# Optimization experiments

Hardware: AMD Instinct MI355X
Metric: run time of the kernel (lower is better)

## Reference

```python
import jax, jax.numpy as jnp
import numpy as np

D_MODEL = 1024
D_FF = 4096
N_EXPERTS = 8
TEMPERATURE = 1.0


def setup_inputs() -> dict:
    key = jax.random.key(0)
    ks = jax.random.split(key, 12)
    s_in = 1.0 / np.sqrt(D_MODEL)
    s_ff = 1.0 / np.sqrt(D_FF)
    return {
        "h": jax.random.normal(ks[0], (2, 2048, D_MODEL), dtype=jnp.float32),
        "Wr": jax.random.normal(ks[1], (D_MODEL, N_EXPERTS), dtype=jnp.float32) * s_in,
        "br": jnp.zeros((N_EXPERTS,), dtype=jnp.float32),
        "We1": jax.random.normal(ks[2], (N_EXPERTS, D_MODEL, D_FF), dtype=jnp.float32) * s_in,
        "be1": jnp.zeros((N_EXPERTS, D_FF), dtype=jnp.float32),
        "We2": jax.random.normal(ks[3], (N_EXPERTS, D_FF, D_MODEL), dtype=jnp.float32) * s_ff,
        "be2": jnp.zeros((N_EXPERTS, D_MODEL), dtype=jnp.float32),
        "Ws1": jax.random.normal(ks[4], (D_MODEL, D_FF), dtype=jnp.float32) * s_in,
        "bs1": jnp.zeros((D_FF,), dtype=jnp.float32),
        "Ws2": jax.random.normal(ks[5], (D_FF, D_MODEL), dtype=jnp.float32) * s_ff,
        "bs2": jnp.zeros((D_MODEL,), dtype=jnp.float32),
        "top_k": 2,
    }


def reference(h, Wr, br, We1, be1, We2, be2, Ws1, bs1, Ws2, bs2, top_k):
    # router: Linear -> temperature-scaled softmax over experts
    gate = jax.nn.softmax((h @ Wr + br) / max(1e-06, TEMPERATURE), axis=-1)  # [b,s,E]
    k = min(int(top_k), gate.shape[-1])
    vals, idx = jax.lax.top_k(gate, k)  # [b,s,k]

    # dense all-expert FFN (matches the original mask-multiply semantics)
    hid = jax.nn.gelu(jnp.einsum('bsd,edf->ebsf', h, We1) + be1[:, None, None, :])
    eout = jnp.einsum('ebsf,efd->ebsd', hid, We2) + be2[:, None, None, :]  # [E,b,s,d]

    # per-expert combine weight: sum over top-k slots of val * onehot(idx)
    onehot = jax.nn.one_hot(idx, gate.shape[-1], dtype=h.dtype)  # [b,s,k,E]
    w_e = jnp.einsum('bsk,bske->bse', vals, onehot)  # [b,s,E]
    out = jnp.einsum('bse,ebsd->bsd', w_e, eout)

    # shared FFN residual branch
    out = out + (jax.nn.gelu(h @ Ws1 + bs1) @ Ws2 + bs2)
    gate_mean = jnp.mean(gate)
    return (out, gate_mean)
```

## Files before the change

### kernel.cpp

```cpp
#include <hip/hip_runtime.h>
#include <hip/hip_bf16.h>
#include <cstdint>
#include <cstddef>

#define NTOK   4096
#define DMODEL 1024
#define DFF    4096
#define NEXP   8
#define ROWCAP 13312
#define MTILES 104

typedef __attribute__((ext_vector_type(8))) short short8;
typedef __attribute__((ext_vector_type(4))) float float4v;

__device__ __forceinline__ unsigned short f2bf(float f) {
    unsigned u = __builtin_bit_cast(unsigned, f);
    u = (u + 0x7fffu + ((u >> 16) & 1u)) >> 16;
    return (unsigned short)u;
}

__device__ __forceinline__ float gelu_f(float x) {
    float u = 0.7978845608028654f * x * (1.f + 0.044715f * x * x);
    float e = __expf(2.f * u);
    return x * (1.f - 1.f / (e + 1.f));
}

__device__ __forceinline__ void gl_lds16(const unsigned short* g, unsigned short* l) {
    __builtin_amdgcn_global_load_lds((const __attribute__((address_space(1))) void*)g,
                                     (__attribute__((address_space(3))) void*)l, 16, 0, 0);
}

__global__ __launch_bounds__(256) void router_k(const float* __restrict__ h,
                                                const float* __restrict__ Wr,
                                                const float* __restrict__ br,
                                                int* __restrict__ meta,
                                                int* __restrict__ slot_e,
                                                int* __restrict__ slot_pos,
                                                float* __restrict__ slot_v,
                                                unsigned short* __restrict__ Xbf,
                                                float* __restrict__ out) {
    __shared__ float wr_s[16 * 516];
    const int tid = threadIdx.x;
    for (int i = tid; i < 8192; i += 256) {
        int j = i >> 3, e = i & 7;
        wr_s[(j >> 6) * 516 + (j & 63) * 8 + e] = Wr[i];
    }
    __syncthreads();
    const int tok = blockIdx.x * 16 + (tid >> 4);
    const int part = tid & 15;
    const float* hp = h + (size_t)tok * DMODEL + part * 64;
    unsigned short* xp = Xbf + (size_t)tok * DMODEL + part * 64;
    const float* wbase = &wr_s[part * 516];
    float acc8[8] = {0.f, 0.f, 0.f, 0.f, 0.f, 0.f, 0.f, 0.f};
    #pragma unroll
    for (int j4 = 0; j4 < 16; j4++) {
        float4v hv = *(const float4v*)(hp + j4 * 4);
        ushort4 o;
        o.x = f2bf(hv[0]); o.y = f2bf(hv[1]); o.z = f2bf(hv[2]); o.w = f2bf(hv[3]);
        *(ushort4*)(xp + j4 * 4) = o;
        #pragma unroll
        for (int jj = 0; jj < 4; jj++) {
            const float* wr = wbase + (j4 * 4 + jj) * 8;
            float4v w0 = *(const float4v*)wr;
            float4v w1 = *(const float4v*)(wr + 4);
            #pragma unroll
            for (int e = 0; e < 4; e++) {
                acc8[e]     = fmaf(hv[jj], w0[e], acc8[e]);
                acc8[e + 4] = fmaf(hv[jj], w1[e], acc8[e + 4]);
            }
        }
    }
    #pragma unroll
    for (int e = 0; e < 8; e++) {
        acc8[e] += __shfl_xor(acc8[e], 1);
        acc8[e] += __shfl_xor(acc8[e], 2);
        acc8[e] += __shfl_xor(acc8[e], 4);
        acc8[e] += __shfl_xor(acc8[e], 8);
    }
    if (part == 0) {
        float p[8];
        float mx = -1e30f;
        #pragma unroll
        for (int e = 0; e < 8; e++) { p[e] = acc8[e] + br[e]; mx = fmaxf(mx, p[e]); }
        float s = 0.f;
        #pragma unroll
        for (int e = 0; e < 8; e++) { p[e] = __expf(p[e] - mx); s += p[e]; }
        float inv = 1.f / s;
        #pragma unroll
        for (int e = 0; e < 8; e++) p[e] *= inv;
        int i1 = 0;
        #pragma unroll
        for (int q = 1; q < 8; q++) if (p[q] > p[i1]) i1 = q;
        int i2 = (i1 == 0) ? 1 : 0;
        #pragma unroll
        for (int q = 0; q < 8; q++) if (q != i1 && p[q] > p[i2]) i2 = q;
        int pos1 = atomicAdd(&meta[i1], 1);
        int pos2 = atomicAdd(&meta[i2], 1);
        slot_e[tok * 2] = i1;     slot_e[tok * 2 + 1] = i2;
        slot_pos[tok * 2] = pos1; slot_pos[tok * 2 + 1] = pos2;
        slot_v[tok * 2] = p[i1];  slot_v[tok * 2 + 1] = p[i2];
    }
    if (blockIdx.x == 0 && tid == 0) out[(size_t)NTOK * DMODEL] = 0.125f;
}

__global__ __launch_bounds__(256) void meta_init(int* __restrict__ meta,
                                                 int* __restrict__ row_token,
                                                 float* __restrict__ row_weight) {
    int i = blockIdx.x * 256 + threadIdx.x;
    if (i < ROWCAP) { row_token[i] = 0; row_weight[i] = 0.f; }
    if (blockIdx.x == 0 && threadIdx.x == 0) {
        int rb = 0;
        meta[8] = 0;
        for (int g = 0; g < 8; g++) {
            rb += ((meta[g] + 127) >> 7) << 7;
            meta[9 + g] = rb;
        }
        meta[17] = rb + NTOK;
    }
}

__global__ __launch_bounds__(256) void scatter_k(const int* __restrict__ meta,
                                                 const int* __restrict__ slot_e,
                                                 const int* __restrict__ slot_pos,
                                                 const float* __restrict__ slot_v,
                                                 int* __restrict__ row_token,
                                                 float* __restrict__ row_weight) {
    int idx = blockIdx.x * 256 + threadIdx.x;
    if (idx < NTOK * 2) {
        int e = slot_e[idx];
        int row = meta[8 + e] + slot_pos[idx];
        row_token[row] = idx >> 1;
        row_weight[row] = slot_v[idx];
    } else if (idx < NTOK * 3) {
        int t = idx - NTOK * 2;
        row_token[meta[16] + t] = t;
        row_weight[meta[16] + t] = 1.0f;
    }
}

__global__ __launch_bounds__(256) void wtrans(const float* __restrict__ Wexp,
                                              const float* __restrict__ Wsh,
                                              unsigned short* __restrict__ dst,
                                              int K, int N) {
    const int g = blockIdx.z;
    const float* src = (g < 8) ? (Wexp + (size_t)g * K * N) : Wsh;
    unsigned short* d = dst + (size_t)g * K * N;
    const int n0 = blockIdx.x * 64, k0 = blockIdx.y * 64;
    __shared__ float t[64 * 65];
    const int r = threadIdx.x >> 4, c4 = (threadIdx.x & 15) * 4;
    #pragma unroll
    for (int i = 0; i < 4; i++) {
        float4v v = *(const float4v*)(src + (size_t)(k0 + r + i * 16) * N + n0 + c4);
        float* tp = &t[(r + i * 16) * 65 + c4];
        tp[0] = v[0]; tp[1] = v[1]; tp[2] = v[2]; tp[3] = v[3];
    }
    __syncthreads();
    const int nn = threadIdx.x >> 3, kc = (threadIdx.x & 7) * 8;
    #pragma unroll
    for (int p = 0; p < 2; p++) {
        int n = p * 32 + nn;
        unsigned short o[8];
        #pragma unroll
        for (int j = 0; j < 8; j++) o[j] = f2bf(t[(kc + j) * 65 + n]);
        *(uint4*)(d + (size_t)(n0 + n) * K + k0 + kc) = *(const uint4*)o;
    }
}

template <int MODE>
__global__ __launch_bounds__(256) void gemm_moe(
    const unsigned short* __restrict__ A,
    const unsigned short* __restrict__ WT,
    const float* __restrict__ bexp,
    const float* __restrict__ bsh,
    unsigned short* __restrict__ HidOut,
    float* __restrict__ Out,
    const int* __restrict__ meta,
    const int* __restrict__ row_token,
    const float* __restrict__ row_weight) {
    constexpr int K = (MODE == 1) ? DMODEL : DFF;
    constexpr int N = (MODE == 1) ? DFF : DMODEL;
    const int n0 = blockIdx.x * 128;
    const int row0 = blockIdx.y * 128;

    __shared__ int rb[10];
    __shared__ unsigned short sm[17408];

    if (threadIdx.x < 10) rb[threadIdx.x] = meta[8 + threadIdx.x];
    __syncthreads();
    if (row0 >= rb[9]) return;
    int g = 0;
    #pragma unroll
    for (int q = 0; q < 8; q++) if (row0 >= rb[q + 1]) g = q + 1;
    const unsigned short* __restrict__ BT = WT + (size_t)g * K * N;
    const float* __restrict__ bias = (g < 8) ? (bexp + (size_t)g * N) : bsh;

    const int tid = threadIdx.x;
    const int wave = tid >> 6, lane = tid & 63;
    const int lrow8 = lane >> 3, kst = lane & 7;
    const int swz = kst ^ lrow8;
    const int wm = wave & 1, wn = wave >> 1;
    const int lr = lane & 15, quad = lane >> 4, l7 = lr & 7;

    const unsigned short* ag[4];
    const unsigned short* bg[4];
    unsigned short* al[4];
    unsigned short* bl[4];
    #pragma unroll
    for (int s = 0; s < 4; s++) {
        int seg = wave * 4 + s;
        int row = seg * 8 + lrow8;
        size_t arow = (MODE == 1) ? (size_t)row_token[row0 + row] : (size_t)(row0 + row);
        ag[s] = A + arow * K + swz * 8;
        bg[s] = BT + (size_t)(n0 + row) * K + swz * 8;
        al[s] = &sm[seg * 512];
        bl[s] = &sm[8192 + seg * 512];
    }

    float4v acc[4][4];
    #pragma unroll
    for (int i = 0; i < 4; i++)
        #pragma unroll
        for (int j = 0; j < 4; j++) acc[i][j] = (float4v){0.f, 0.f, 0.f, 0.f};

    for (int kb = 0; kb < K; kb += 64) {
        #pragma unroll
        for (int s = 0; s < 4; s++) gl_lds16(ag[s] + kb, al[s]);
        #pragma unroll
        for (int s = 0; s < 4; s++) gl_lds16(bg[s] + kb, bl[s]);
        __syncthreads();
        #pragma unroll
        for (int ks = 0; ks < 2; ks++) {
            const int koff = ((ks * 4 + quad) ^ l7) * 8;
            short8 af[4], bf[4];
            #pragma unroll
            for (int mi = 0; mi < 4; mi++)
                af[mi] = *(const short8*)&sm[(wm * 64 + mi * 16 + lr) * 64 + koff];
            #pragma unroll
            for (int ni = 0; ni < 4; ni++)
                bf[ni] = *(const short8*)&sm[8192 + (wn * 64 + ni * 16 + lr) * 64 + koff];
            #pragma unroll
            for (int mi = 0; mi < 4; mi++)
                #pragma unroll
                for (int ni = 0; ni < 4; ni++)
                    acc[mi][ni] = __builtin_amdgcn_mfma_f32_16x16x32_bf16(
                        af[mi], bf[ni], acc[mi][ni], 0, 0, 0);
        }
        __syncthreads();
    }

    if (MODE == 1) {
        #pragma unroll
        for (int ni = 0; ni < 4; ni++) {
            int col = wn * 64 + ni * 16 + lr;
            float b = bias[n0 + col];
            #pragma unroll
            for (int mi = 0; mi < 4; mi++) {
                int rowb = wm * 64 + mi * 16 + quad * 4;
                #pragma unroll
                for (int r2 = 0; r2 < 4; r2++)
                    sm[(rowb + r2) * 136 + col] = f2bf(gelu_f(acc[mi][ni][r2] + b));
            }
        }
        __syncthreads();
        const int row = tid >> 1, half = tid & 1;
        const unsigned short* srcp = &sm[row * 136 + half * 64];
        unsigned short* dstp = &HidOut[(size_t)(row0 + row) * DFF + n0 + half * 64];
        #pragma unroll
        for (int j = 0; j < 8; j++)
            *(uint4*)(dstp + j * 8) = *(const uint4*)(srcp + j * 8);
    } else {
        #pragma unroll
        for (int mi = 0; mi < 4; mi++) {
            int rbase = row0 + wm * 64 + mi * 16 + quad * 4;
            int tok[4]; float w[4];
            #pragma unroll
            for (int r2 = 0; r2 < 4; r2++) {
                tok[r2] = row_token[rbase + r2];
                w[r2] = row_weight[rbase + r2];
            }
            #pragma unroll
            for (int ni = 0; ni < 4; ni++) {
                int col = n0 + wn * 64 + ni * 16 + lr;
                float b = bias[col];
                #pragma unroll
                for (int r2 = 0; r2 < 4; r2++) {
                    if (w[r2] != 0.f)
                        atomicAdd(&Out[(size_t)tok[r2] * DMODEL + col],
                                  w[r2] * (acc[mi][ni][r2] + b));
                }
            }
        }
    }
}

extern "C" void kernel_launch(void* const* d_in, const int* in_sizes, int n_in,
                              void* d_out, int out_size, void* d_ws, size_t ws_size,
                              hipStream_t stream) {
    const float* h   = (const float*)d_in[0];
    const float* Wr  = (const float*)d_in[1];
    const float* br  = (const float*)d_in[2];
    const float* We1 = (const float*)d_in[3];
    const float* be1 = (const float*)d_in[4];
    const float* We2 = (const float*)d_in[5];
    const float* be2 = (const float*)d_in[6];
    const float* Ws1 = (const float*)d_in[7];
    const float* bs1 = (const float*)d_in[8];
    const float* Ws2 = (const float*)d_in[9];
    const float* bs2 = (const float*)d_in[10];
    float* out = (float*)d_out;

    char* ws = (char*)d_ws;
    int* meta         = (int*)ws;
    int* slot_e       = (int*)(ws + 4096);
    int* slot_pos     = (int*)(ws + 36864);
    float* slot_v     = (float*)(ws + 69632);
    int* row_token    = (int*)(ws + 102400);
    float* row_weight = (float*)(ws + 155648);
    unsigned short* Xbf = (unsigned short*)(ws + (1ull << 20));
    unsigned short* WT  = (unsigned short*)(ws + (16ull << 20));
    unsigned short* Hid = (unsigned short*)(ws + (96ull << 20));

    hipMemsetAsync(meta, 0, 256, stream);
    hipMemsetAsync(d_out, 0, sizeof(float) * (size_t)out_size, stream);
    router_k<<<NTOK / 16, 256, 0, stream>>>(h, Wr, br, meta, slot_e, slot_pos, slot_v, Xbf, out);
    meta_init<<<ROWCAP / 256, 256, 0, stream>>>(meta, row_token, row_weight);
    scatter_k<<<(NTOK * 3) / 256, 256, 0, stream>>>(meta, slot_e, slot_pos, slot_v,
                                                    row_token, row_weight);
    wtrans<<<dim3(DFF / 64, DMODEL / 64, 9), 256, 0, stream>>>(We1, Ws1, WT, DMODEL, DFF);
    gemm_moe<1><<<dim3(DFF / 128, MTILES), 256, 0, stream>>>(
        Xbf, WT, be1, bs1, Hid, nullptr, meta, row_token, row_weight);
    wtrans<<<dim3(DMODEL / 64, DFF / 64, 9), 256, 0, stream>>>(We2, Ws2, WT, DFF, DMODEL);
    gemm_moe<2><<<dim3(DMODEL / 128, MTILES), 256, 0, stream>>>(
        Hid, WT, be2, bs2, nullptr, out, meta, row_token, row_weight);
}
```

Baseline: 779.2 us.

## Load GEMM fragments directly from global with panel-packed weights and split-K

Result: slower. 1.310 ms (+68.1%).

```diff
diff --git a/kernel.cpp b/kernel.cpp
--- a/kernel.cpp
+++ b/kernel.cpp
@@ -23,11 +23,6 @@
     float u = 0.7978845608028654f * x * (1.f + 0.044715f * x * x);
     float e = __expf(2.f * u);
     return x * (1.f - 1.f / (e + 1.f));
-}
-
-__device__ __forceinline__ void gl_lds16(const unsigned short* g, unsigned short* l) {
-    __builtin_amdgcn_global_load_lds((const __attribute__((address_space(1))) void*)g,
-                                     (__attribute__((address_space(3))) void*)l, 16, 0, 0);
 }
 
 __global__ __launch_bounds__(256) void router_k(const float* __restrict__ h,
@@ -156,18 +151,19 @@
     }
     __syncthreads();
     const int nn = threadIdx.x >> 3, kc = (threadIdx.x & 7) * 8;
+    unsigned short* dpan = d + (size_t)(k0 >> 6) * ((size_t)N * 64);
     #pragma unroll
     for (int p = 0; p < 2; p++) {
         int n = p * 32 + nn;
         unsigned short o[8];
         #pragma unroll
         for (int j = 0; j < 8; j++) o[j] = f2bf(t[(kc + j) * 65 + n]);
-        *(uint4*)(d + (size_t)(n0 + n) * K + k0 + kc) = *(const uint4*)o;
+        *(uint4*)(dpan + (size_t)(n0 + n) * 64 + kc) = *(const uint4*)o;
     }
 }
 
 template <int MODE>
-__global__ __launch_bounds__(256) void gemm_moe(
+__global__ __launch_bounds__(256, 2) void gemm_moe(
     const unsigned short* __restrict__ A,
     const unsigned short* __restrict__ WT,
     const float* __restrict__ bexp,
@@ -179,11 +175,14 @@
     const float* __restrict__ row_weight) {
     constexpr int K = (MODE == 1) ? DMODEL : DFF;
     constexpr int N = (MODE == 1) ? DFF : DMODEL;
+    constexpr int KCHUNK = (MODE == 1) ? DMODEL : (DFF / 2);
     const int n0 = blockIdx.x * 128;
     const int row0 = blockIdx.y * 128;
+    const int kz0 = blockIdx.z * KCHUNK;
 
     __shared__ int rb[10];
-    __shared__ unsigned short sm[17408];
+    constexpr int CEL = (MODE == 1) ? (128 * 136) : 16;
+    __shared__ unsigned short sm[CEL];
 
     if (threadIdx.x < 10) rb[threadIdx.x] = meta[8 + threadIdx.x];
     __syncthreads();
@@ -196,24 +195,21 @@
 
     const int tid = threadIdx.x;
     const int wave = tid >> 6, lane = tid & 63;
-    const int lrow8 = lane >> 3, kst = lane & 7;
-    const int swz = kst ^ lrow8;
     const int wm = wave & 1, wn = wave >> 1;
-    const int lr = lane & 15, quad = lane >> 4, l7 = lr & 7;
-
-    const unsigned short* ag[4];
-    const unsigned short* bg[4];
-    unsigned short* al[4];
-    unsigned short* bl[4];
-    #pragma unroll
-    for (int s = 0; s < 4; s++) {
-        int seg = wave * 4 + s;
-        int row = seg * 8 + lrow8;
-        size_t arow = (MODE == 1) ? (size_t)row_token[row0 + row] : (size_t)(row0 + row);
-        ag[s] = A + arow * K + swz * 8;
-        bg[s] = BT + (size_t)(n0 + row) * K + swz * 8;
-        al[s] = &sm[seg * 512];
-        bl[s] = &sm[8192 + seg * 512];
+    const int lr = lane & 15, quad = lane >> 4;
+
+    const unsigned short* ap[4];
+    const unsigned short* bp[4];
+    #pragma unroll
+    for (int mi = 0; mi < 4; mi++) {
+        int m = row0 + wm * 64 + mi * 16 + lr;
+        size_t arow = (MODE == 1) ? (size_t)row_token[m] : (size_t)m;
+        ap[mi] = A + arow * K + kz0 + quad * 8;
+    }
+    #pragma unroll
+    for (int ni = 0; ni < 4; ni++) {
+        int n = n0 + wn * 64 + ni * 16 + lr;
+        bp[ni] = BT + (size_t)(kz0 >> 6) * ((size_t)N * 64) + (size_t)n * 64 + quad * 8;
     }
 
     float4v acc[4][4];
@@ -222,30 +218,26 @@
         #pragma unroll
         for (int j = 0; j < 4; j++) acc[i][j] = (float4v){0.f, 0.f, 0.f, 0.f};
 
-    for (int kb = 0; kb < K; kb += 64) {
-        #pragma unroll
-        for (int s = 0; s < 4; s++) gl_lds16(ag[s] + kb, al[s]);
-        #pragma unroll
-        for (int s = 0; s < 4; s++) gl_lds16(bg[s] + kb, bl[s]);
-        __syncthreads();
-        #pragma unroll
-        for (int ks = 0; ks < 2; ks++) {
-            const int koff = ((ks * 4 + quad) ^ l7) * 8;
-            short8 af[4], bf[4];
+    for (int kb = 0; kb < KCHUNK; kb += 64) {
+        short8 af[2][4], bf[2][4];
+        #pragma unroll
+        for (int ks = 0; ks < 2; ks++)
             #pragma unroll
             for (int mi = 0; mi < 4; mi++)
-                af[mi] = *(const short8*)&sm[(wm * 64 + mi * 16 + lr) * 64 + koff];
+                af[ks][mi] = *(const short8*)(ap[mi] + kb + ks * 32);
+        #pragma unroll
+        for (int ks = 0; ks < 2; ks++)
             #pragma unroll
             for (int ni = 0; ni < 4; ni++)
-                bf[ni] = *(const short8*)&sm[8192 + (wn * 64 + ni * 16 + lr) * 64 + koff];
+                bf[ks][ni] = *(const short8*)(bp[ni] + (size_t)kb * N + ks * 32);
+        #pragma unroll
+        for (int ks = 0; ks < 2; ks++)
             #pragma unroll
             for (int mi = 0; mi < 4; mi++)
                 #pragma unroll
                 for (int ni = 0; ni < 4; ni++)
                     acc[mi][ni] = __builtin_amdgcn_mfma_f32_16x16x32_bf16(
-                        af[mi], bf[ni], acc[mi][ni], 0, 0, 0);
-        }
-        __syncthreads();
+                        af[ks][mi], bf[ks][ni], acc[mi][ni], 0, 0, 0);
     }
 
     if (MODE == 1) {
@@ -269,6 +261,7 @@
         for (int j = 0; j < 8; j++)
             *(uint4*)(dstp + j * 8) = *(const uint4*)(srcp + j * 8);
     } else {
+        const bool addb = (kz0 == 0);
         #pragma unroll
         for (int mi = 0; mi < 4; mi++) {
             int rbase = row0 + wm * 64 + mi * 16 + quad * 4;
@@ -281,7 +274,7 @@
             #pragma unroll
             for (int ni = 0; ni < 4; ni++) {
                 int col = n0 + wn * 64 + ni * 16 + lr;
-                float b = bias[col];
+                float b = addb ? bias[col] : 0.f;
                 #pragma unroll
                 for (int r2 = 0; r2 < 4; r2++) {
                     if (w[r2] != 0.f)
@@ -330,6 +323,6 @@
     gemm_moe<1><<<dim3(DFF / 128, MTILES), 256, 0, stream>>>(
         Xbf, WT, be1, bs1, Hid, nullptr, meta, row_token, row_weight);
     wtrans<<<dim3(DMODEL / 64, DFF / 64, 9), 256, 0, stream>>>(We2, Ws2, WT, DFF, DMODEL);
-    gemm_moe<2><<<dim3(DMODEL / 128, MTILES), 256, 0, stream>>>(
+    gemm_moe<2><<<dim3(DMODEL / 128, MTILES, 2), 256, 0, stream>>>(
         Hid, WT, be2, bs2, nullptr, out, meta, row_token, row_weight);
 }
```
